# Optimization experiments

Hardware: AMD Instinct MI355X
Metric: run time of the kernel (lower is better)

Reference implementation:

```python
import jax, jax.numpy as jnp
import numpy as np

V, E, D, T, B = 32000, 512, 512, 512, 32
PAD = 3

def layer_norm(x, g, b, eps=1e-5):
    m = jnp.mean(x, axis=-1, keepdims=True)
    v = jnp.mean((x - m) ** 2, axis=-1, keepdims=True)
    return (x - m) * jax.lax.rsqrt(v + eps) * g + b

def sru_direction(U, v, b, reverse):
    # U: (T, B, 4D) -> splits: x_tilde, f-gate pre-act, r-gate pre-act, highway input
    x_t, uf, ur, xp = jnp.split(U, 4, axis=-1)
    def step(c, inp):
        xt, uft, urt, xpt = inp
        f = jax.nn.sigmoid(uft + v[0] * c + b[0])
        r = jax.nn.sigmoid(urt + v[1] * c + b[1])
        c_new = f * c + (1.0 - f) * xt
        h = r * c_new + (1.0 - r) * xpt
        return c_new, h
    c0 = jnp.zeros((U.shape[1], v.shape[1]), U.dtype)  # (B, D)
    c_last, hs = jax.lax.scan(step, c0, (x_t, uf, ur, xp), reverse=reverse)
    return hs, c_last

def setup_inputs() -> dict:
    key = jax.random.key(0)
    ks = jax.random.split(key, 8)
    def rn(k, shp, sc=0.05):
        return jax.random.normal(k, shp, jnp.float32) * sc
    return {
        "src": jax.random.randint(ks[0], (T, B), 0, V),
        "emb": rn(ks[1], (V, E), 0.1),
        "ln_g": jnp.ones((E,), jnp.float32),
        "ln_b": jnp.zeros((E,), jnp.float32),
        "W0": rn(ks[2], (E, 4 * D)),
        "W1": rn(ks[3], (E, 4 * D)),
        "v0": rn(ks[4], (2, D), 0.5),
        "v1": rn(ks[5], (2, D), 0.5),
        "b0": jnp.zeros((2, D), jnp.float32),
        "b1": jnp.zeros((2, D), jnp.float32),
        "W_out": rn(ks[6], (D, 2 * D)),
        "b_out": jnp.zeros((D,), jnp.float32),
    }

def reference(src, emb, ln_g, ln_b, W0, W1, v0, v1, b0, b1, W_out, b_out):
    table = emb.at[PAD].set(0.0)          # padding_idx row is zero
    x = table[src]                         # (T, B, E); dropout p=0 -> identity
    xn = layer_norm(x, ln_g, ln_b)         # SRU layer_norm=True: LN on cell input
    h0, c0 = sru_direction(jnp.einsum('tbe,ef->tbf', xn, W0), v0, b0, False)
    h1, c1 = sru_direction(jnp.einsum('tbe,ef->tbf', xn, W1), v1, b1, True)
    outputs = jnp.concatenate([h0, h1], axis=-1)        # (T, B, 2D)
    hidden = jnp.concatenate([c0, c1], axis=-1)[None]   # (1, B, 2D)
    out = jnp.tanh(jnp.einsum('tbh,dh->tbd', outputs, W_out) + b_out)
    return out, hidden
```

## Files before the change

kernel.cpp:

```cpp
#include <hip/hip_runtime.h>
#include <cstdint>
#include <cstddef>

#define T_DIM 512
#define B_DIM 32
#define E_DIM 512
#define D_DIM 512
#define PAD_IDX 3
#define M_ROWS (T_DIM * B_DIM)
#define PF 32

typedef __attribute__((ext_vector_type(8))) __bf16 bf16x8;
typedef __attribute__((ext_vector_type(4))) float  f32x4;

__device__ __forceinline__ unsigned short f2bf(float x) {
    union { float f; uint32_t u; } v; v.f = x;
    uint32_t u = v.u;
    uint32_t r = (u + 0x7FFFu + ((u >> 16) & 1u)) >> 16;
    return (unsigned short)r;
}
__device__ __forceinline__ float bf2f(unsigned short h) {
    union { float f; uint32_t u; } v; v.u = ((uint32_t)h) << 16;
    return v.f;
}
__device__ __forceinline__ float fast_sigmoid(float z) {
    return __builtin_amdgcn_rcpf(1.f + __expf(-z));
}
__device__ __forceinline__ float fast_tanh(float x) {
    return 1.f - 2.f * __builtin_amdgcn_rcpf(__expf(2.f * x) + 1.f);
}

__global__ __launch_bounds__(256) void wconv_kernel(
    const float* __restrict__ W0, const float* __restrict__ W1,
    unsigned short* __restrict__ Wt)
{
    __shared__ float tile[64][65];
    int k0  = blockIdx.x * 64;
    int n0g = blockIdx.y * 64;
    int dir = n0g >> 11;
    const float* W = dir ? W1 : W0;
    int d0 = (n0g & 2047) >> 2;
    int tx = threadIdx.x & 63;
    int ty = threadIdx.x >> 6;
    int scol = ((tx >> 4) << 9) + d0 + (tx & 15);
    for (int r = ty; r < 64; r += 4)
        tile[r][tx] = W[(size_t)(k0 + r) * 2048 + scol];
    __syncthreads();
    for (int r2 = ty; r2 < 64; r2 += 4) {
        int j = ((r2 & 3) << 4) | (r2 >> 2);
        Wt[(size_t)(n0g + r2) * 512 + k0 + tx] = f2bf(tile[tx][j]);
    }
}

__global__ __launch_bounds__(256) void bias_build_kernel(
    const float* __restrict__ b0, const float* __restrict__ b1,
    float* __restrict__ bias)
{
    int n = blockIdx.x * 256 + threadIdx.x;
    int dir = n >> 11, g = n & 3, d = (n & 2047) >> 2;
    const float* bp = dir ? b1 : b0;
    float v = (g == 1) ? bp[d] : ((g == 2) ? bp[512 + d] : 0.f);
    bias[n] = v;
}

__global__ __launch_bounds__(256) void woutconv_kernel(
    const float* __restrict__ W, unsigned short* __restrict__ O)
{
    int i = (blockIdx.x * 256 + threadIdx.x) * 4;
    f32x4 v = *(const f32x4*)(W + i);
    uint2 pk;
    pk.x = (uint32_t)f2bf(v[0]) | ((uint32_t)f2bf(v[1]) << 16);
    pk.y = (uint32_t)f2bf(v[2]) | ((uint32_t)f2bf(v[3]) << 16);
    *(uint2*)(O + i) = pk;
}

__global__ __launch_bounds__(256) void embed_ln_kernel(
    const int* __restrict__ src, const float* __restrict__ emb,
    const float* __restrict__ g, const float* __restrict__ bb,
    unsigned short* __restrict__ xn)
{
    int wave = threadIdx.x >> 6;
    int lane = threadIdx.x & 63;
    int row  = blockIdx.x * 4 + wave;
    int tok  = src[row];
    float x[8];
    if (tok == PAD_IDX) {
        #pragma unroll
        for (int j = 0; j < 8; j++) x[j] = 0.f;
    } else {
        const float* er = emb + (size_t)tok * E_DIM + lane * 8;
        f32x4 a0 = *(const f32x4*)(er);
        f32x4 a1 = *(const f32x4*)(er + 4);
        #pragma unroll
        for (int j = 0; j < 4; j++) { x[j] = a0[j]; x[4 + j] = a1[j]; }
    }
    float s = 0.f, sq = 0.f;
    #pragma unroll
    for (int j = 0; j < 8; j++) { s += x[j]; sq += x[j] * x[j]; }
    #pragma unroll
    for (int off = 32; off >= 1; off >>= 1) {
        s  += __shfl_xor(s,  off, 64);
        sq += __shfl_xor(sq, off, 64);
    }
    float mean = s * (1.f / 512.f);
    float var  = sq * (1.f / 512.f) - mean * mean;
    float rs   = rsqrtf(var + 1e-5f);
    f32x4 g0 = *(const f32x4*)(g + lane * 8);
    f32x4 g1 = *(const f32x4*)(g + lane * 8 + 4);
    f32x4 b0 = *(const f32x4*)(bb + lane * 8);
    f32x4 b1 = *(const f32x4*)(bb + lane * 8 + 4);
    unsigned short o[8];
    #pragma unroll
    for (int j = 0; j < 4; j++) {
        o[j]     = f2bf((x[j]     - mean) * rs * g0[j] + b0[j]);
        o[4 + j] = f2bf((x[4 + j] - mean) * rs * g1[j] + b1[j]);
    }
    uint4 pk;
    pk.x = (uint32_t)o[0] | ((uint32_t)o[1] << 16);
    pk.y = (uint32_t)o[2] | ((uint32_t)o[3] << 16);
    pk.z = (uint32_t)o[4] | ((uint32_t)o[5] << 16);
    pk.w = (uint32_t)o[6] | ((uint32_t)o[7] << 16);
    *(uint4*)(xn + (size_t)row * E_DIM + lane * 8) = pk;
}

template<int KD, int NMT, int NNT, int GM, int GN, int EPI>
__global__ __launch_bounds__(512, 4) void gemm_pipe_kernel(
    const unsigned short* __restrict__ A,
    const unsigned short* __restrict__ Bt,
    void* __restrict__ Cout,
    const float* __restrict__ bias,
    int ldc)
{
    constexpr int BM = 128, BN = 256;
    constexpr int MR = 4, NR = 4;
    constexpr int NKT = KD / 32;
    constexpr int RA  = BM / 128;
    constexpr int RB  = BN / 128;
    constexpr int LPT = RA + RB;
    constexpr int ASZ = BM * 32;
    constexpr int BSZ = BN * 32;
    __shared__ unsigned short smem[3 * (ASZ + BSZ)];

    const int tid = threadIdx.x;
    const int w   = tid >> 6;
    const int l   = tid & 63;

    constexpr int PER_G = GM * GN;
    constexpr int NGC   = NNT / GN;
    const int bid = blockIdx.x;
    const int c   = bid & 7;
    const int idx = bid >> 3;
    const int gi  = idx / PER_G;
    const int wi  = idx % PER_G;
    const int gg  = c + 8 * gi;
    const int mt  = (gg / NGC) * GM + wi / GN;
    const int nt  = (gg % NGC) * GN + wi % GN;

    const int wm = w >> 2, wn = w & 3;

    const unsigned short* Ab = A  + (size_t)mt * BM * KD;
    const unsigned short* Bb = Bt + (size_t)nt * BN * KD;

    const int srow = w * 16 + (l >> 2);
    const int scol = ((l & 3) ^ ((l >> 3) & 3)) * 8;

    auto stage = [&](int t, int slot) {
        const unsigned short* Ag = Ab + t * 32;
        const unsigned short* Bg = Bb + t * 32;
        unsigned short* As = smem + slot * (ASZ + BSZ);
        unsigned short* Bs = As + ASZ;
        #pragma unroll
        for (int r = 0; r < RA; r++)
            __builtin_amdgcn_global_load_lds(
                (const __attribute__((address_space(1))) void*)(Ag + (size_t)(r * 128 + srow) * KD + scol),
                (__attribute__((address_space(3))) void*)(As + (r * 128 + w * 16) * 32),
                16, 0, 0);
        #pragma unroll
        for (int r = 0; r < RB; r++)
            __builtin_amdgcn_global_load_lds(
                (const __attribute__((address_space(1))) void*)(Bg + (size_t)(r * 128 + srow) * KD + scol),
                (__attribute__((address_space(3))) void*)(Bs + (r * 128 + w * 16) * 32),
                16, 0, 0);
    };

    f32x4 acc[MR][NR];
    #pragma unroll
    for (int m = 0; m < MR; m++)
        #pragma unroll
        for (int n = 0; n < NR; n++)
            acc[m][n] = (f32x4){0.f, 0.f, 0.f, 0.f};

    stage(0, 0); stage(1, 1);

    const int li   = l & 15;
    const int cg   = l >> 4;
    const int rswz = (cg ^ ((li >> 1) & 3)) * 8;

    int rs = 0, ss = 2;
    for (int t = 0; t < NKT; t++) {
        if (t + 1 < NKT)
            asm volatile("s_waitcnt vmcnt(%0) lgkmcnt(0)" :: "n"(LPT) : "memory");
        else
            asm volatile("s_waitcnt vmcnt(0) lgkmcnt(0)" ::: "memory");
        __builtin_amdgcn_s_barrier();
        if (t + 2 < NKT) stage(t + 2, ss);

        const unsigned short* As = smem + rs * (ASZ + BSZ);
        const unsigned short* Bs = As + ASZ;
        bf16x8 af[MR], bfv[NR];
        #pragma unroll
        for (int m = 0; m < MR; m++) {
            int row = wm * 64 + m * 16 + li;
            af[m] = *(const bf16x8*)(As + row * 32 + rswz);
        }
        #pragma unroll
        for (int n = 0; n < NR; n++) {
            int row = wn * 64 + n * 16 + li;
            bfv[n] = *(const bf16x8*)(Bs + row * 32 + rswz);
        }
        __builtin_amdgcn_s_setprio(1);
        #pragma unroll
        for (int m = 0; m < MR; m++)
            #pragma unroll
            for (int n = 0; n < NR; n++)
                acc[m][n] = __builtin_amdgcn_mfma_f32_16x16x32_bf16(
                    af[m], bfv[n], acc[m][n], 0, 0, 0);
        __builtin_amdgcn_s_setprio(0);

        rs = (rs == 2) ? 0 : rs + 1;
        ss = (ss == 2) ? 0 : ss + 1;
    }

    const int colb = nt * BN + wn * 64;
    const int rowb = mt * BM + wm * 64;
    #pragma unroll
    for (int m = 0; m < MR; m++) {
        #pragma unroll
        for (int n = 0; n < NR; n++) {
            int col  = colb + n * 16 + li;
            int row0 = rowb + m * 16 + cg * 4;
            float bi = bias[col];
            if (EPI == 0) {
                unsigned short* C = (unsigned short*)Cout;
                #pragma unroll
                for (int j = 0; j < 4; j++)
                    C[(size_t)(row0 + j) * ldc + col] = f2bf(acc[m][n][j] + bi);
            } else {
                float* C = (float*)Cout;
                #pragma unroll
                for (int j = 0; j < 4; j++)
                    C[(size_t)(row0 + j) * ldc + col] = fast_tanh(acc[m][n][j] + bi);
            }
        }
    }
}

__global__ __launch_bounds__(64) void sru_scan_kernel(
    const unsigned short* __restrict__ U,
    const float* __restrict__ v0, const float* __restrict__ v1,
    unsigned short* __restrict__ h,
    float* __restrict__ hidden)
{
    int id  = blockIdx.x * 64 + threadIdx.x;
    int dir = id >> 14;
    int rem = id & 16383;
    int b   = rem >> 9;
    int d   = rem & 511;
    const float* v = dir ? v1 : v0;
    float vf = v[d], vr = v[D_DIM + d];

    int row0  = (dir ? (T_DIM - 1) * B_DIM : 0) + b;
    long step = (long)(dir ? -B_DIM : B_DIM) * 1024;

    const ushort4* lp = (const ushort4*)U + (size_t)row0 * 1024 + dir * 512 + d;
    unsigned short* hp = h + (size_t)row0 * 1024 + dir * 512 + d;

    ushort4 buf[PF];
    #pragma unroll
    for (int p = 0; p < PF; p++) { buf[p] = *lp; lp += step; }

    float c = 0.f;
    for (int tb = 0; tb < T_DIM - PF; tb += PF) {
        #pragma unroll
        for (int p = 0; p < PF; p++) {
            ushort4 q = buf[p];
            buf[p] = *lp; lp += step;
            float x  = bf2f(q.x);
            float uf = bf2f(q.y);
            float ur = bf2f(q.z);
            float xp = bf2f(q.w);
            float f = fast_sigmoid(__fmaf_rn(vf, c, uf));
            float r = fast_sigmoid(__fmaf_rn(vr, c, ur));
            c = __fmaf_rn(f, c - x, x);
            float hv = __fmaf_rn(r, c - xp, xp);
            *hp = f2bf(hv); hp += step;
        }
    }
    #pragma unroll
    for (int p = 0; p < PF; p++) {
        ushort4 q = buf[p];
        float x  = bf2f(q.x);
        float uf = bf2f(q.y);
        float ur = bf2f(q.z);
        float xp = bf2f(q.w);
        float f = fast_sigmoid(__fmaf_rn(vf, c, uf));
        float r = fast_sigmoid(__fmaf_rn(vr, c, ur));
        c = __fmaf_rn(f, c - x, x);
        float hv = __fmaf_rn(r, c - xp, xp);
        *hp = f2bf(hv); hp += step;
    }
    hidden[b * 1024 + dir * 512 + d] = c;
}

extern "C" void kernel_launch(void* const* d_in, const int* in_sizes, int n_in,
                              void* d_out, int out_size, void* d_ws, size_t ws_size,
                              hipStream_t stream)
{
    const int*   src   = (const int*)  d_in[0];
    const float* emb   = (const float*)d_in[1];
    const float* ln_g  = (const float*)d_in[2];
    const float* ln_b  = (const float*)d_in[3];
    const float* W0    = (const float*)d_in[4];
    const float* W1    = (const float*)d_in[5];
    const float* v0    = (const float*)d_in[6];
    const float* v1    = (const float*)d_in[7];
    const float* b0    = (const float*)d_in[8];
    const float* b1    = (const float*)d_in[9];
    const float* W_out = (const float*)d_in[10];
    const float* b_out = (const float*)d_in[11];

    unsigned short* Wt  = (unsigned short*)d_ws;
    unsigned short* Wob = Wt  + (size_t)4096 * 512;
    unsigned short* xn  = Wob + (size_t)512 * 1024;
    unsigned short* U   = xn  + (size_t)M_ROWS * 512;
    unsigned short* h   = U   + (size_t)M_ROWS * 4096;
    float*          bias4096 = (float*)(h + (size_t)M_ROWS * 1024);

    float* out    = (float*)d_out;
    float* hidden = out + (size_t)M_ROWS * D_DIM;
    (void)out;

    wconv_kernel<<<dim3(8, 64), 256, 0, stream>>>(W0, W1, Wt);
    bias_build_kernel<<<16, 256, 0, stream>>>(b0, b1, bias4096);
    woutconv_kernel<<<512, 256, 0, stream>>>(W_out, Wob);
    embed_ln_kernel<<<M_ROWS / 4, 256, 0, stream>>>(src, emb, ln_g, ln_b, xn);

    gemm_pipe_kernel<512, 128, 16, 8, 4, 0>
        <<<2048, 512, 0, stream>>>(xn, Wt, (void*)U, bias4096, 4096);

    sru_scan_kernel<<<512, 64, 0, stream>>>(U, v0, v1, h, hidden);

    gemm_pipe_kernel<1024, 128, 2, 8, 2, 1>
        <<<256, 512, 0, stream>>>(h, Wob, (void*)d_out, b_out, 512);
}
```

Measured before the change: 163.2 us.

## Replace input GEMM with 256x256-tile eight-phase pipelined MFMA kernel

Adds a new GEMM kernel using 256x256 output tiles with a K-step of 64. It double-buffers through 128KB of LDS via direct global-to-LDS loads and interleaves half-tile loads with four MFMA phases per K step, using barriers and setprio. It replaces the 128x256-tile kernel for the large xn·W projection, aiming at more data reuse per tile and better overlap of loads with compute. The cost is higher register and LDS pressure, which leaves only one or two blocks per CU, and a grid of 1024 blocks.

Measured after the change: 172.0 us. +5.4%, slower.

```diff
diff --git a/kernel.cpp b/kernel.cpp
--- a/kernel.cpp
+++ b/kernel.cpp
@@ -121,6 +121,152 @@
     pk.z = (uint32_t)o[4] | ((uint32_t)o[5] << 16);
     pk.w = (uint32_t)o[6] | ((uint32_t)o[7] << 16);
     *(uint4*)(xn + (size_t)row * E_DIM + lane * 8) = pk;
+}
+
+template<int KD, int NMT, int NNT, int GM, int GN, int EPI>
+__global__ __launch_bounds__(512, 2) void gemm8p_kernel(
+    const unsigned short* __restrict__ A,
+    const unsigned short* __restrict__ Bt,
+    void* __restrict__ Cout,
+    const float* __restrict__ bias,
+    int ldc)
+{
+    constexpr int NT = KD / 64;
+    __shared__ unsigned short smem[65536];
+
+    const int tid = threadIdx.x;
+    const int w   = tid >> 6;
+    const int l   = tid & 63;
+    const int li  = l & 15;
+    const int cg  = l >> 4;
+    const int rf  = ((l >> 2) & 1) << 4;
+
+    constexpr int PER_G = GM * GN;
+    constexpr int NGC   = NNT / GN;
+    const int bid = blockIdx.x;
+    const int c   = bid & 7;
+    const int idx = bid >> 3;
+    const int gi  = idx / PER_G;
+    const int wi  = idx % PER_G;
+    const int gg  = c + 8 * gi;
+    const int mt  = (gg / NGC) * GM + wi / GN;
+    const int nt  = (gg % NGC) * GN + wi % GN;
+
+    const int wm = w >> 2, wn = w & 3;
+
+    const unsigned short* Ab = A  + (size_t)mt * 256 * KD;
+    const unsigned short* Bb = Bt + (size_t)nt * 256 * KD;
+
+    const int s_colx = ((l & 7) * 8) ^ (((l >> 5) & 1) << 4);
+    const int s_rl   = w * 8 + (l >> 3);
+
+    auto stage_half = [&](int tt, int mat, int mh) {
+        const unsigned short* G = (mat ? Bb : Ab) + (size_t)(mh * 128 + s_rl) * KD + tt * 64 + s_colx;
+        unsigned short* D = smem + (tt & 1) * 32768 + mat * 16384 + mh * 8192 + w * 512;
+        __builtin_amdgcn_global_load_lds(
+            (const __attribute__((address_space(1))) void*)(G),
+            (__attribute__((address_space(3))) void*)(D), 16, 0, 0);
+        __builtin_amdgcn_global_load_lds(
+            (const __attribute__((address_space(1))) void*)(G + (size_t)64 * KD),
+            (__attribute__((address_space(3))) void*)(D + 8 * 512), 16, 0, 0);
+    };
+
+    f32x4 acc[8][4];
+    #pragma unroll
+    for (int m = 0; m < 8; m++)
+        #pragma unroll
+        for (int n = 0; n < 4; n++)
+            acc[m][n] = (f32x4){0.f, 0.f, 0.f, 0.f};
+
+    stage_half(0, 1, 0); stage_half(0, 0, 0); stage_half(0, 1, 1); stage_half(0, 0, 1);
+    stage_half(1, 1, 0); stage_half(1, 0, 0); stage_half(1, 1, 1);
+    asm volatile("s_waitcnt vmcnt(6)" ::: "memory");
+    __builtin_amdgcn_s_barrier();
+
+    bf16x8 af[4][2], bf[4][2];
+
+#define READ_A(MH)                                                             \
+    _Pragma("unroll")                                                          \
+    for (int m2 = 0; m2 < 4; m2++)                                             \
+        _Pragma("unroll")                                                      \
+        for (int ks = 0; ks < 2; ks++)                                         \
+            af[m2][ks] = *(const bf16x8*)(As + (wm * 128 + ((MH) * 4 + m2) * 16 + li) * 64 \
+                                          + ((ks * 32 + cg * 8) ^ rf));
+#define READ_B(NH)                                                             \
+    _Pragma("unroll")                                                          \
+    for (int n2 = 0; n2 < 2; n2++)                                             \
+        _Pragma("unroll")                                                      \
+        for (int ks = 0; ks < 2; ks++)                                         \
+            bf[(NH) * 2 + n2][ks] = *(const bf16x8*)(Bs + (wn * 64 + ((NH) * 2 + n2) * 16 + li) * 64 \
+                                          + ((ks * 32 + cg * 8) ^ rf));
+#define PH_MFMA(MH, NH)                                                        \
+    __builtin_amdgcn_s_barrier();                                              \
+    asm volatile("s_waitcnt lgkmcnt(0)" ::: "memory");                         \
+    __builtin_amdgcn_sched_barrier(0);                                         \
+    __builtin_amdgcn_s_setprio(1);                                             \
+    _Pragma("unroll")                                                          \
+    for (int m2 = 0; m2 < 4; m2++)                                             \
+        _Pragma("unroll")                                                      \
+        for (int n2 = 0; n2 < 2; n2++)                                         \
+            _Pragma("unroll")                                                  \
+            for (int ks = 0; ks < 2; ks++)                                     \
+                acc[(MH) * 4 + m2][(NH) * 2 + n2] =                            \
+                    __builtin_amdgcn_mfma_f32_16x16x32_bf16(                   \
+                        af[m2][ks], bf[(NH) * 2 + n2][ks],                     \
+                        acc[(MH) * 4 + m2][(NH) * 2 + n2], 0, 0, 0);           \
+    __builtin_amdgcn_s_setprio(0);                                             \
+    __builtin_amdgcn_sched_barrier(0);
+
+    #pragma unroll 2
+    for (int t = 0; t < NT; t++) {
+        const unsigned short* As = smem + (t & 1) * 32768;
+        const unsigned short* Bs = As + 16384;
+        READ_A(0); READ_B(0);
+        if (t + 1 < NT) stage_half(t + 1, 0, 1);
+        PH_MFMA(0, 0);
+        __builtin_amdgcn_s_barrier();
+        READ_B(1);
+        if (t + 2 < NT) stage_half(t + 2, 1, 0);
+        PH_MFMA(0, 1);
+        __builtin_amdgcn_s_barrier();
+        READ_A(1);
+        if (t + 2 < NT) stage_half(t + 2, 0, 0);
+        PH_MFMA(1, 0);
+        __builtin_amdgcn_s_barrier();
+        if (t + 2 < NT) stage_half(t + 2, 1, 1);
+        PH_MFMA(1, 1);
+        if (t + 1 < NT) {
+            if (t + 2 < NT) { asm volatile("s_waitcnt vmcnt(6)" ::: "memory"); }
+            else            { asm volatile("s_waitcnt vmcnt(0)" ::: "memory"); }
+        }
+        __builtin_amdgcn_s_barrier();
+    }
+#undef READ_A
+#undef READ_B
+#undef PH_MFMA
+
+    const int colb = nt * 256 + wn * 64;
+    const int rowb = mt * 256 + wm * 128;
+    #pragma unroll
+    for (int m = 0; m < 8; m++) {
+        #pragma unroll
+        for (int n = 0; n < 4; n++) {
+            int col  = colb + n * 16 + li;
+            int row0 = rowb + m * 16 + cg * 4;
+            float bi = bias[col];
+            if (EPI == 0) {
+                unsigned short* C = (unsigned short*)Cout;
+                #pragma unroll
+                for (int j = 0; j < 4; j++)
+                    C[(size_t)(row0 + j) * ldc + col] = f2bf(acc[m][n][j] + bi);
+            } else {
+                float* C = (float*)Cout;
+                #pragma unroll
+                for (int j = 0; j < 4; j++)
+                    C[(size_t)(row0 + j) * ldc + col] = fast_tanh(acc[m][n][j] + bi);
+            }
+        }
+    }
 }
 
 template<int KD, int NMT, int NNT, int GM, int GN, int EPI>
@@ -345,8 +491,8 @@
     woutconv_kernel<<<512, 256, 0, stream>>>(W_out, Wob);
     embed_ln_kernel<<<M_ROWS / 4, 256, 0, stream>>>(src, emb, ln_g, ln_b, xn);
 
-    gemm_pipe_kernel<512, 128, 16, 8, 4, 0>
-        <<<2048, 512, 0, stream>>>(xn, Wt, (void*)U, bias4096, 4096);
+    gemm8p_kernel<512, 64, 16, 4, 2, 0>
+        <<<1024, 512, 0, stream>>>(xn, Wt, (void*)U, bias4096, 4096);
 
     sru_scan_kernel<<<512, 64, 0, stream>>>(U, v0, v1, h, hidden);
 
```

## Restructure GEMM to 4-wave blocks with 8 M-fragments per wave

Applied to the files above, without the earlier changes.

Replaces the 8-wave 128x256 GEMM with a 4-wave kernel in which each wave covers all 128 rows (8 MFMA row fragments) and a BN/4 column strip, which raises register-level reuse of the B fragments. The output GEMM now uses a 128x128 tile with 512 blocks instead of 256 for more parallelism, and the block swizzle and occupancy hints are retuned. The cost is higher accumulator register pressure and fewer waves per block to hide latency.

Measured after the change: 168.2 us. 1.03x slower.

```diff
diff --git a/kernel.cpp b/kernel.cpp
--- a/kernel.cpp
+++ b/kernel.cpp
@@ -123,21 +123,18 @@
     *(uint4*)(xn + (size_t)row * E_DIM + lane * 8) = pk;
 }
 
-template<int KD, int NMT, int NNT, int GM, int GN, int EPI>
-__global__ __launch_bounds__(512, 4) void gemm_pipe_kernel(
+template<int KD, int BN, int NMT, int NNT, int GM, int GN, int OCC, int EPI>
+__global__ __launch_bounds__(256, OCC) void gemm_mr8_kernel(
     const unsigned short* __restrict__ A,
     const unsigned short* __restrict__ Bt,
     void* __restrict__ Cout,
     const float* __restrict__ bias,
     int ldc)
 {
-    constexpr int BM = 128, BN = 256;
-    constexpr int MR = 4, NR = 4;
     constexpr int NKT = KD / 32;
-    constexpr int RA  = BM / 128;
-    constexpr int RB  = BN / 128;
-    constexpr int LPT = RA + RB;
-    constexpr int ASZ = BM * 32;
+    constexpr int NR  = BN / 64;
+    constexpr int LPT = 2 + NR;
+    constexpr int ASZ = 128 * 32;
     constexpr int BSZ = BN * 32;
     __shared__ unsigned short smem[3 * (ASZ + BSZ)];
 
@@ -156,36 +153,38 @@
     const int mt  = (gg / NGC) * GM + wi / GN;
     const int nt  = (gg % NGC) * GN + wi % GN;
 
-    const int wm = w >> 2, wn = w & 3;
-
-    const unsigned short* Ab = A  + (size_t)mt * BM * KD;
+    const unsigned short* Ab = A  + (size_t)mt * 128 * KD;
     const unsigned short* Bb = Bt + (size_t)nt * BN * KD;
 
-    const int srow = w * 16 + (l >> 2);
-    const int scol = ((l & 3) ^ ((l >> 3) & 3)) * 8;
+    const int s_colx = (((l & 3) ^ ((l >> 3) & 3)) * 8);
+    const int s_row  = l >> 2;
 
     auto stage = [&](int t, int slot) {
-        const unsigned short* Ag = Ab + t * 32;
-        const unsigned short* Bg = Bb + t * 32;
         unsigned short* As = smem + slot * (ASZ + BSZ);
         unsigned short* Bs = As + ASZ;
-        #pragma unroll
-        for (int r = 0; r < RA; r++)
+        const unsigned short* Ag = Ab + t * 32 + s_colx;
+        const unsigned short* Bg = Bb + t * 32 + s_colx;
+        #pragma unroll
+        for (int i = 0; i < 2; i++) {
+            int g = w * 2 + i;
             __builtin_amdgcn_global_load_lds(
-                (const __attribute__((address_space(1))) void*)(Ag + (size_t)(r * 128 + srow) * KD + scol),
-                (__attribute__((address_space(3))) void*)(As + (r * 128 + w * 16) * 32),
+                (const __attribute__((address_space(1))) void*)(Ag + (size_t)(g * 16 + s_row) * KD),
+                (__attribute__((address_space(3))) void*)(As + g * 512),
                 16, 0, 0);
-        #pragma unroll
-        for (int r = 0; r < RB; r++)
+        }
+        #pragma unroll
+        for (int j = 0; j < NR; j++) {
+            int g = w * NR + j;
             __builtin_amdgcn_global_load_lds(
-                (const __attribute__((address_space(1))) void*)(Bg + (size_t)(r * 128 + srow) * KD + scol),
-                (__attribute__((address_space(3))) void*)(Bs + (r * 128 + w * 16) * 32),
+                (const __attribute__((address_space(1))) void*)(Bg + (size_t)(g * 16 + s_row) * KD),
+                (__attribute__((address_space(3))) void*)(Bs + g * 512),
                 16, 0, 0);
+        }
     };
 
-    f32x4 acc[MR][NR];
-    #pragma unroll
-    for (int m = 0; m < MR; m++)
+    f32x4 acc[8][NR];
+    #pragma unroll
+    for (int m = 0; m < 8; m++)
         #pragma unroll
         for (int n = 0; n < NR; n++)
             acc[m][n] = (f32x4){0.f, 0.f, 0.f, 0.f};
@@ -207,20 +206,20 @@
 
         const unsigned short* As = smem + rs * (ASZ + BSZ);
         const unsigned short* Bs = As + ASZ;
-        bf16x8 af[MR], bfv[NR];
-        #pragma unroll
-        for (int m = 0; m < MR; m++) {
-            int row = wm * 64 + m * 16 + li;
+        bf16x8 af[8], bfv[NR];
+        #pragma unroll
+        for (int m = 0; m < 8; m++) {
+            int row = m * 16 + li;
             af[m] = *(const bf16x8*)(As + row * 32 + rswz);
         }
         #pragma unroll
         for (int n = 0; n < NR; n++) {
-            int row = wn * 64 + n * 16 + li;
+            int row = w * (NR * 16) + n * 16 + li;
             bfv[n] = *(const bf16x8*)(Bs + row * 32 + rswz);
         }
         __builtin_amdgcn_s_setprio(1);
         #pragma unroll
-        for (int m = 0; m < MR; m++)
+        for (int m = 0; m < 8; m++)
             #pragma unroll
             for (int n = 0; n < NR; n++)
                 acc[m][n] = __builtin_amdgcn_mfma_f32_16x16x32_bf16(
@@ -231,10 +230,10 @@
         ss = (ss == 2) ? 0 : ss + 1;
     }
 
-    const int colb = nt * BN + wn * 64;
-    const int rowb = mt * BM + wm * 64;
-    #pragma unroll
-    for (int m = 0; m < MR; m++) {
+    const int colb = nt * BN + w * (NR * 16);
+    const int rowb = mt * 128;
+    #pragma unroll
+    for (int m = 0; m < 8; m++) {
         #pragma unroll
         for (int n = 0; n < NR; n++) {
             int col  = colb + n * 16 + li;
@@ -345,11 +344,11 @@
     woutconv_kernel<<<512, 256, 0, stream>>>(W_out, Wob);
     embed_ln_kernel<<<M_ROWS / 4, 256, 0, stream>>>(src, emb, ln_g, ln_b, xn);
 
-    gemm_pipe_kernel<512, 128, 16, 8, 4, 0>
-        <<<2048, 512, 0, stream>>>(xn, Wt, (void*)U, bias4096, 4096);
+    gemm_mr8_kernel<512, 256, 128, 16, 8, 2, 2, 0>
+        <<<2048, 256, 0, stream>>>(xn, Wt, (void*)U, bias4096, 4096);
 
     sru_scan_kernel<<<512, 64, 0, stream>>>(U, v0, v1, h, hidden);
 
-    gemm_pipe_kernel<1024, 128, 2, 8, 2, 1>
-        <<<256, 512, 0, stream>>>(h, Wob, (void*)d_out, b_out, 512);
-}
+    gemm_mr8_kernel<1024, 128, 128, 4, 8, 2, 3, 1>
+        <<<512, 256, 0, stream>>>(h, Wob, (void*)d_out, b_out, 512);
+}
```
